# Optimization experiments

Measured on AMD Instinct MI355X. Metric: run time of the kernel, lower is better.

Reference implementation:

```python
import jax, jax.numpy as jnp
import numpy as np

B = 16384
OBS = 568        # 36 self features + 19 * 28 other-agent features
H = 256          # hidden_dim
SELF_DIM = 36
OTHER_DIM = 28
N_OTHER = (OBS - SELF_DIM) // OTHER_DIM  # 19


def _linear_init(key, fan_in, fan_out):
    # torch nn.Linear default: U(-1/sqrt(fan_in), 1/sqrt(fan_in))
    kw, kb = jax.random.split(key)
    s = 1.0 / np.sqrt(fan_in)
    W = jax.random.uniform(kw, (fan_in, fan_out), jnp.float32, -s, s)
    b = jax.random.uniform(kb, (fan_out,), jnp.float32, -s, s)
    return W, b


def setup_inputs() -> dict:
    key = jax.random.key(0)
    ks = jax.random.split(key, 10)
    x = jax.random.normal(ks[0], (B, OBS), jnp.float32)
    eps = jax.random.normal(ks[1], (B, H), jnp.float32)
    W_mu, b_mu = _linear_init(ks[2], OBS, H)
    W_var, b_var = _linear_init(ks[3], OBS, H)
    W_self, b_self = _linear_init(ks[4], SELF_DIM, H)
    W_other, b_other = _linear_init(ks[5], OTHER_DIM, H)
    W_q, b_q = _linear_init(ks[6], H, H)
    W_k, b_k = _linear_init(ks[7], H, H)
    W_v, b_v = _linear_init(ks[8], 2 * H, H)
    W_a, b_a = _linear_init(ks[9], 2 * H, H)
    return {"x": x, "eps": eps,
            "W_mu": W_mu, "b_mu": b_mu, "W_var": W_var, "b_var": b_var,
            "W_self": W_self, "b_self": b_self, "W_other": W_other, "b_other": b_other,
            "W_q": W_q, "b_q": b_q, "W_k": W_k, "b_k": b_k,
            "W_v": W_v, "b_v": b_v, "W_a": W_a, "b_a": b_a}


def reference(x, eps, W_mu, b_mu, W_var, b_var, W_self, b_self,
              W_other, b_other, W_q, b_q, W_k, b_k, W_v, b_v, W_a, b_a):
    relu = jax.nn.relu
    # VAE reparameterization (detach=False path)
    mu = x @ W_mu + b_mu                                  # [B, H]
    log_var = x @ W_var + b_var                           # [B, H]
    z = eps * jnp.exp(0.5 * log_var) + mu                 # [B, H]

    self_info = x[:, :SELF_DIM]                           # [B, 36]
    agents_info = x[:, SELF_DIM:].reshape(B, N_OTHER, OTHER_DIM)  # [B, N, 28]

    self_em = relu(self_info @ W_self + b_self)           # [B, H]
    other_ems = relu(agents_info @ W_other + b_other)     # [B, N, H]

    q = relu(z @ W_q + b_q)                               # [B, H]
    k = relu(other_ems @ W_k + b_k)                       # [B, N, H]
    v_in = jnp.concatenate(
        [other_ems, jnp.broadcast_to(self_em[:, None, :], (B, N_OTHER, H))], axis=-1)
    v = relu(v_in @ W_v + b_v)                            # [B, N, H]

    scores = jnp.einsum('bh,bnh->bn', q, k) / np.sqrt(H)  # [B, N]
    att_weight = jax.nn.softmax(scores, axis=-1)          # [B, N]
    h = jnp.einsum('bn,bnh->bh', att_weight, v)           # [B, H]

    out = relu(jnp.concatenate([h, self_em], axis=-1) @ W_a + b_a)  # [B, H]
    return out, att_weight[:, None, :]                    # att: [B, 1, N]
```

## Files before the change

### kernel.cpp

```cpp
#include <hip/hip_runtime.h>

typedef __bf16 bf16;
typedef __bf16 bf16x4 __attribute__((ext_vector_type(4)));
typedef __bf16 bf16x8 __attribute__((ext_vector_type(8)));
typedef float  f32x4  __attribute__((ext_vector_type(4)));

#define NB    16384
#define NOBS  568
#define NH    256
#define NAG   19

#define OFF_WT_MU    0u
#define OFF_WT_VAR   294912u
#define OFF_WT_SELF  589824u
#define OFF_WT_OTHER 622592u
#define OFF_WT_Q     638976u
#define OFF_WT_K     770048u
#define OFF_WT_V1    901120u
#define OFF_WT_V2    1032192u
#define OFF_WT_A1    1163264u
#define OFF_WT_A2    1294336u
#define OFF_Z        1425408u
#define OFF_SELF     9814016u
#define OFF_Q        18202624u
#define OFF_SV       26591232u
#define OFF_H        34979840u

static __device__ __forceinline__ unsigned short bfbits(float v) {
  bf16 b = (bf16)v;
  union { bf16 b; unsigned short u; } cvt; cvt.b = b; return cvt.u;
}

__global__ __launch_bounds__(256) void wprep(
    const float* __restrict__ Wmu, const float* __restrict__ Wvar,
    const float* __restrict__ Wself, const float* __restrict__ Wother,
    const float* __restrict__ Wq, const float* __restrict__ Wk,
    const float* __restrict__ Wv, const float* __restrict__ Wa, char* wsb)
{
  const float* src; bf16* dst; int K, Kp; bool chunked = false;
  switch (blockIdx.y) {
    case 0: src = Wmu;        dst = (bf16*)(wsb + OFF_WT_MU);    K = 568; Kp = 576; break;
    case 1: src = Wvar;       dst = (bf16*)(wsb + OFF_WT_VAR);   K = 568; Kp = 576; break;
    case 2: src = Wself;      dst = (bf16*)(wsb + OFF_WT_SELF);  K = 36;  Kp = 64;  break;
    case 3: src = Wother;     dst = (bf16*)(wsb + OFF_WT_OTHER); K = 28;  Kp = 32;  break;
    case 4: src = Wq;         dst = (bf16*)(wsb + OFF_WT_Q);     K = 256; Kp = 256; break;
    case 5: src = Wk;         dst = (bf16*)(wsb + OFF_WT_K);     K = 256; Kp = 256; chunked = true; break;
    case 6: src = Wv;         dst = (bf16*)(wsb + OFF_WT_V1);    K = 256; Kp = 256; chunked = true; break;
    case 7: src = Wv + 65536; dst = (bf16*)(wsb + OFF_WT_V2);    K = 256; Kp = 256; break;
    case 8: src = Wa;         dst = (bf16*)(wsb + OFF_WT_A1);    K = 256; Kp = 256; break;
    default: src = Wa + 65536; dst = (bf16*)(wsb + OFF_WT_A2);   K = 256; Kp = 256; break;
  }
  int total = 256 * Kp;
  if (chunked) {
    for (int i = blockIdx.x * 256 + threadIdx.x; i < total; i += gridDim.x * 256) {
      int ch = i >> 13, n = (i >> 5) & 255, kk = i & 31;
      int k = ch * 32 + kk;
      dst[i] = (bf16)src[k * 256 + n];
    }
  } else {
    for (int i = blockIdx.x * 256 + threadIdx.x; i < total; i += gridDim.x * 256) {
      int n = i / Kp, k = i - n * Kp;
      dst[i] = (k < K) ? (bf16)src[k * 256 + n] : (bf16)0.f;
    }
  }
}

template<int EMODE, bool AF32>
__global__ __launch_bounds__(256, 2) void gemm_k(
    const void* __restrict__ Aptr, const void* __restrict__ A2ptr,
    int lda, int K, int Klimit,
    const bf16* __restrict__ Wt, const bf16* __restrict__ Wt2,
    const float* __restrict__ bias, const float* __restrict__ bias2,
    const float* __restrict__ epsp, void* __restrict__ outp)
{
  constexpr bool DUALB = (EMODE == 0);
  constexpr bool DUALA = (EMODE == 3);
  __shared__ bf16 ldsA[64 * 40];
  __shared__ bf16 ldsB[128 * 40];
  __shared__ bf16 ldsB2[DUALB ? 128 * 40 : 8];

  const int tid = threadIdx.x;
  const int wave = tid >> 6;
  const int lane = tid & 63;
  const int quad = lane >> 4;
  const int m = lane & 15;
  const int rowbase = blockIdx.x * 64;
  const int colbase = blockIdx.y * 128;

  f32x4 acc[8];
  f32x4 accB[DUALB ? 8 : 1];
  const f32x4 z4 = {0.f, 0.f, 0.f, 0.f};
#pragma unroll
  for (int ct = 0; ct < 8; ++ct) acc[ct] = z4;
  if constexpr (DUALB) {
#pragma unroll
    for (int ct = 0; ct < 8; ++ct) accB[ct] = z4;
  }

  const int npass = DUALA ? 2 : 1;
  for (int pass = 0; pass < npass; ++pass) {
    const void* Ap = (pass == 0) ? Aptr : A2ptr;
    const bf16* Wp = (pass == 0) ? Wt : Wt2;
    for (int kc = 0; kc < K; kc += 32) {
      __syncthreads();
      if constexpr (AF32) {
        const float* Af = (const float*)Ap;
#pragma unroll
        for (int it = 0; it < 2; ++it) {
          int p = tid + 256 * it;
          int r = p >> 3, fs = p & 7;
          int k = kc + fs * 4;
          const float* src = Af + (size_t)(rowbase + r) * lda + k;
          float v0, v1, v2, v3;
          if (k + 4 <= Klimit) {
            float4 v = *(const float4*)src;
            v0 = v.x; v1 = v.y; v2 = v.z; v3 = v.w;
          } else {
            v0 = (k + 0 < Klimit) ? src[0] : 0.f;
            v1 = (k + 1 < Klimit) ? src[1] : 0.f;
            v2 = (k + 2 < Klimit) ? src[2] : 0.f;
            v3 = (k + 3 < Klimit) ? src[3] : 0.f;
          }
          bf16x4 o = {(bf16)v0, (bf16)v1, (bf16)v2, (bf16)v3};
          *(bf16x4*)(ldsA + r * 40 + fs * 4) = o;
        }
      } else {
        const bf16* Ab = (const bf16*)Ap;
        {
          int p = tid;
          int r = p >> 2, f = p & 3;
          *(bf16x8*)(ldsA + r * 40 + f * 8) =
              *(const bf16x8*)(Ab + (size_t)(rowbase + r) * lda + kc + f * 8);
        }
      }
#pragma unroll
      for (int it = 0; it < 2; ++it) {
        int p = tid + 256 * it;
        int n = p >> 2, f = p & 3;
        *(bf16x8*)(ldsB + n * 40 + f * 8) =
            *(const bf16x8*)(Wt + (size_t)(colbase + n) * K + kc + f * 8);
      }
      if constexpr (DUALB) {
#pragma unroll
        for (int it = 0; it < 2; ++it) {
          int p = tid + 256 * it;
          int n = p >> 2, f = p & 3;
          *(bf16x8*)(ldsB2 + n * 40 + f * 8) =
              *(const bf16x8*)(Wt2 + (size_t)(colbase + n) * K + kc + f * 8);
        }
      }
      __syncthreads();
      bf16x8 afrag = *(const bf16x8*)(ldsA + (wave * 16 + m) * 40 + quad * 8);
#pragma unroll
      for (int ct = 0; ct < 8; ++ct) {
        bf16x8 bfrag = *(const bf16x8*)(ldsB + (ct * 16 + m) * 40 + quad * 8);
        acc[ct] = __builtin_amdgcn_mfma_f32_16x16x32_bf16(afrag, bfrag, acc[ct], 0, 0, 0);
        if constexpr (DUALB) {
          bf16x8 b2 = *(const bf16x8*)(ldsB2 + (ct * 16 + m) * 40 + quad * 8);
          accB[ct] = __builtin_amdgcn_mfma_f32_16x16x32_bf16(afrag, b2, accB[ct], 0, 0, 0);
        }
      }
      (void)Wp;
    }
  }
#pragma unroll
  for (int ct = 0; ct < 8; ++ct) {
    const int col = colbase + ct * 16 + m;
    const float bv = bias[col];
#pragma unroll
    for (int r = 0; r < 4; ++r) {
      const size_t row = (size_t)rowbase + wave * 16 + quad * 4 + r;
      float v = acc[ct][r] + bv;
      if constexpr (EMODE == 0) {
        float lv = accB[ct][r] + bias2[col];
        float zz = epsp[row * 256 + col] * __expf(0.5f * lv) + v;
        ((bf16*)outp)[row * 256 + col] = (bf16)zz;
      } else if constexpr (EMODE == 1) {
        ((bf16*)outp)[row * 256 + col] = (bf16)(v > 0.f ? v : 0.f);
      } else if constexpr (EMODE == 2) {
        ((bf16*)outp)[row * 256 + col] = (bf16)v;
      } else {
        ((float*)outp)[row * 256 + col] = (v > 0.f ? v : 0.f);
      }
    }
  }
}

template<bool UNUSED>
__global__ __launch_bounds__(256, 2) void gemm_dualA(
    const bf16* __restrict__ A1, const bf16* __restrict__ A2,
    const bf16* __restrict__ Wt1, const bf16* __restrict__ Wt2,
    const float* __restrict__ bias, float* __restrict__ outp)
{
  __shared__ bf16 ldsA[64 * 40];
  __shared__ bf16 ldsB[128 * 40];

  const int tid = threadIdx.x;
  const int wave = tid >> 6;
  const int lane = tid & 63;
  const int quad = lane >> 4;
  const int m = lane & 15;
  const int rowbase = blockIdx.x * 64;
  const int colbase = blockIdx.y * 128;

  f32x4 acc[8];
  const f32x4 z4 = {0.f, 0.f, 0.f, 0.f};
#pragma unroll
  for (int ct = 0; ct < 8; ++ct) acc[ct] = z4;

  for (int pass = 0; pass < 2; ++pass) {
    const bf16* Ap = (pass == 0) ? A1 : A2;
    const bf16* Wp = (pass == 0) ? Wt1 : Wt2;
    for (int kc = 0; kc < 256; kc += 32) {
      __syncthreads();
      {
        int p = tid;
        int r = p >> 2, f = p & 3;
        *(bf16x8*)(ldsA + r * 40 + f * 8) =
            *(const bf16x8*)(Ap + (size_t)(rowbase + r) * 256 + kc + f * 8);
      }
#pragma unroll
      for (int it = 0; it < 2; ++it) {
        int p = tid + 256 * it;
        int n = p >> 2, f = p & 3;
        *(bf16x8*)(ldsB + n * 40 + f * 8) =
            *(const bf16x8*)(Wp + (size_t)(colbase + n) * 256 + kc + f * 8);
      }
      __syncthreads();
      bf16x8 afrag = *(const bf16x8*)(ldsA + (wave * 16 + m) * 40 + quad * 8);
#pragma unroll
      for (int ct = 0; ct < 8; ++ct) {
        bf16x8 bfrag = *(const bf16x8*)(ldsB + (ct * 16 + m) * 40 + quad * 8);
        acc[ct] = __builtin_amdgcn_mfma_f32_16x16x32_bf16(afrag, bfrag, acc[ct], 0, 0, 0);
      }
    }
  }
#pragma unroll
  for (int ct = 0; ct < 8; ++ct) {
    const int col = colbase + ct * 16 + m;
    const float bv = bias[col];
#pragma unroll
    for (int r = 0; r < 4; ++r) {
      const size_t row = (size_t)rowbase + wave * 16 + quad * 4 + r;
      float v = acc[ct][r] + bv;
      outp[row * 256 + col] = (v > 0.f ? v : 0.f);
    }
  }
}

__global__ __launch_bounds__(256, 3) void k_fused(
    const float* __restrict__ x, const bf16* __restrict__ qb,
    const bf16* __restrict__ svb,
    const bf16* __restrict__ WtOther, const float* __restrict__ b_other,
    const bf16* __restrict__ WtKc, const float* __restrict__ b_k,
    const bf16* __restrict__ WtVc,
    float* __restrict__ att_out, bf16* __restrict__ hb)
{
  __shared__ bf16 ldsO[80 * 264];
  __shared__ bf16 ldsA1[80 * 40];
  __shared__ bf16 qh16[1024];
  __shared__ bf16 svl16[1024];
  float* spart = (float*)ldsA1;
  float* attl  = (float*)ldsA1 + 320;

  const int tid = threadIdx.x, wave = tid >> 6, lane = tid & 63;
  const int quad = lane >> 4, m = lane & 15;
  const int b0 = blockIdx.x * 4;

  for (int i = tid; i < 512; i += 256) {
    ((unsigned*)qh16)[i]  = ((const unsigned*)(qb  + (size_t)b0 * 256))[i];
    ((unsigned*)svl16)[i] = ((const unsigned*)(svb + (size_t)b0 * 256))[i];
  }
  for (int i = tid; i < 80 * 16; i += 256) {
    int r = i >> 4, kk = (i & 15) * 2;
    float v0 = 0.f, v1 = 0.f;
    if (r < 76) {
      int bb = b0 + r / 19, n = r % 19;
      const float* base = x + (size_t)bb * NOBS + 36 + n * 28;
      if (kk < 28) v0 = base[kk];
      if (kk + 1 < 28) v1 = base[kk + 1];
    }
    unsigned u0 = bfbits(v0), u1 = bfbits(v1);
    *(unsigned*)(ldsA1 + r * 40 + kk) = u0 | (u1 << 16);
  }
  __syncthreads();

  const f32x4 z4 = {0.f, 0.f, 0.f, 0.f};

  {
    f32x4 acc1[5][4];
    bf16x8 bfr[4];
#pragma unroll
    for (int c = 0; c < 4; ++c)
      bfr[c] = *(const bf16x8*)(WtOther + ((4 * wave + c) * 16 + m) * 32 + quad * 8);
#pragma unroll
    for (int rt = 0; rt < 5; ++rt) {
      bf16x8 a = *(const bf16x8*)(ldsA1 + (rt * 16 + m) * 40 + quad * 8);
#pragma unroll
      for (int c = 0; c < 4; ++c)
        acc1[rt][c] = __builtin_amdgcn_mfma_f32_16x16x32_bf16(a, bfr[c], z4, 0, 0, 0);
    }
#pragma unroll
    for (int rt = 0; rt < 5; ++rt)
#pragma unroll
      for (int c = 0; c < 4; ++c) {
        int col = (4 * wave + c) * 16 + m;
        float bv = b_other[col];
#pragma unroll
        for (int r = 0; r < 4; ++r) {
          float v = acc1[rt][c][r] + bv;
          v = v > 0.f ? v : 0.f;
          unsigned u = bfbits(v);
          unsigned other = (unsigned)__shfl_xor((int)u, 1, 64);
          if ((m & 1) == 0) {
            int rowl = rt * 16 + quad * 4 + r;
            *(unsigned*)(ldsO + rowl * 264 + col) = u | (other << 16);
          }
        }
      }
  }
  __syncthreads();

  {
    f32x4 aK[5][4];
#pragma unroll
    for (int rt = 0; rt < 5; ++rt)
#pragma unroll
      for (int c = 0; c < 4; ++c) aK[rt][c] = z4;

#pragma unroll 1
    for (int ch = 0; ch < 8; ++ch) {
      const int kc = ch * 32;
      bf16x8 bK[4];
#pragma unroll
      for (int c = 0; c < 4; ++c)
        bK[c] = *(const bf16x8*)(WtKc + (size_t)ch * 8192 + ((4 * wave + c) * 16 + m) * 32 + quad * 8);
#pragma unroll
      for (int rt = 0; rt < 5; ++rt) {
        bf16x8 a = *(const bf16x8*)(ldsO + (rt * 16 + m) * 264 + kc + quad * 8);
#pragma unroll
        for (int c = 0; c < 4; ++c)
          aK[rt][c] = __builtin_amdgcn_mfma_f32_16x16x32_bf16(a, bK[c], aK[rt][c], 0, 0, 0);
      }
    }

#pragma unroll
    for (int rt = 0; rt < 5; ++rt) {
      float part[4] = {0.f, 0.f, 0.f, 0.f};
#pragma unroll
      for (int c = 0; c < 4; ++c) {
        int col = (4 * wave + c) * 16 + m;
        float bkv = b_k[col];
#pragma unroll
        for (int r = 0; r < 4; ++r) {
          int rowl = rt * 16 + quad * 4 + r;
          int br = rowl / 19; int bs = br > 3 ? 3 : br;
          float kv = aK[rt][c][r] + bkv;
          kv = kv > 0.f ? kv : 0.f;
          part[r] += kv * (float)qh16[bs * 256 + col];
        }
      }
#pragma unroll
      for (int r = 0; r < 4; ++r) {
        float p = part[r];
        p += __shfl_xor(p, 1, 64);
        p += __shfl_xor(p, 2, 64);
        p += __shfl_xor(p, 4, 64);
        p += __shfl_xor(p, 8, 64);
        if (m == 0) spart[wave * 80 + rt * 16 + quad * 4 + r] = p;
      }
    }
  }
  __syncthreads();
  if (tid < 4) {
    float sc[19];
    float mx = -1e30f;
#pragma unroll
    for (int j = 0; j < 19; ++j) {
      int row = tid * 19 + j;
      float s = (spart[row] + spart[80 + row] + spart[160 + row] + spart[240 + row]) * 0.0625f;
      sc[j] = s; mx = fmaxf(mx, s);
    }
    float sum = 0.f;
#pragma unroll
    for (int j = 0; j < 19; ++j) { float e = __expf(sc[j] - mx); sc[j] = e; sum += e; }
    float inv = 1.f / sum;
#pragma unroll
    for (int j = 0; j < 19; ++j) {
      float a = sc[j] * inv;
      attl[tid * 19 + j] = a;
      att_out[(size_t)(b0 + tid) * 19 + j] = a;
    }
  }
  __syncthreads();

  {
    f32x4 aV[5][4];
#pragma unroll
    for (int rt = 0; rt < 5; ++rt)
#pragma unroll
      for (int c = 0; c < 4; ++c) aV[rt][c] = z4;

#pragma unroll 1
    for (int ch = 0; ch < 8; ++ch) {
      const int kc = ch * 32;
      bf16x8 bV[4];
#pragma unroll
      for (int c = 0; c < 4; ++c)
        bV[c] = *(const bf16x8*)(WtVc + (size_t)ch * 8192 + ((4 * wave + c) * 16 + m) * 32 + quad * 8);
#pragma unroll
      for (int rt = 0; rt < 5; ++rt) {
        bf16x8 a = *(const bf16x8*)(ldsO + (rt * 16 + m) * 264 + kc + quad * 8);
#pragma unroll
        for (int c = 0; c < 4; ++c)
          aV[rt][c] = __builtin_amdgcn_mfma_f32_16x16x32_bf16(a, bV[c], aV[rt][c], 0, 0, 0);
      }
    }

    float hacc[4][4];
#pragma unroll
    for (int c = 0; c < 4; ++c)
#pragma unroll
      for (int bb = 0; bb < 4; ++bb) hacc[c][bb] = 0.f;
#pragma unroll
    for (int rt = 0; rt < 5; ++rt)
#pragma unroll
      for (int c = 0; c < 4; ++c) {
        int col = (4 * wave + c) * 16 + m;
#pragma unroll
        for (int r = 0; r < 4; ++r) {
          int rowl = rt * 16 + quad * 4 + r;
          int br = rowl / 19; int bs = br > 3 ? 3 : br;
          float v = aV[rt][c][r] + (float)svl16[bs * 256 + col];
          v = v > 0.f ? v : 0.f;
          int ai = bs * 19 + (rowl - bs * 19);
          float hv = v * attl[ai < 76 ? ai : 75];
#pragma unroll
          for (int bb = 0; bb < 4; ++bb)
            hacc[c][bb] += (br == bb) ? hv : 0.f;
        }
      }
    __syncthreads();
#pragma unroll
    for (int c = 0; c < 4; ++c)
#pragma unroll
      for (int bb = 0; bb < 4; ++bb) {
        float h = hacc[c][bb];
        h += __shfl_xor(h, 16, 64);
        h += __shfl_xor(h, 32, 64);
        if (quad == 0) qh16[bb * 256 + (4 * wave + c) * 16 + m] = (bf16)h;
      }
  }
  __syncthreads();
  for (int i = tid; i < 512; i += 256)
    ((unsigned*)(hb + (size_t)b0 * 256))[i] = ((const unsigned*)qh16)[i];
}

extern "C" void kernel_launch(void* const* d_in, const int* in_sizes, int n_in,
                              void* d_out, int out_size, void* d_ws, size_t ws_size,
                              hipStream_t stream) {
  (void)in_sizes; (void)n_in; (void)out_size; (void)ws_size;
  const float* x      = (const float*)d_in[0];
  const float* eps    = (const float*)d_in[1];
  const float* W_mu   = (const float*)d_in[2];
  const float* b_mu   = (const float*)d_in[3];
  const float* W_var  = (const float*)d_in[4];
  const float* b_var  = (const float*)d_in[5];
  const float* W_self = (const float*)d_in[6];
  const float* b_self = (const float*)d_in[7];
  const float* W_other= (const float*)d_in[8];
  const float* b_other= (const float*)d_in[9];
  const float* W_q    = (const float*)d_in[10];
  const float* b_q    = (const float*)d_in[11];
  const float* W_k    = (const float*)d_in[12];
  const float* b_k    = (const float*)d_in[13];
  const float* W_v    = (const float*)d_in[14];
  const float* b_v    = (const float*)d_in[15];
  const float* W_a    = (const float*)d_in[16];
  const float* b_a    = (const float*)d_in[17];

  char* wsb = (char*)d_ws;
  bf16* WtMu    = (bf16*)(wsb + OFF_WT_MU);
  bf16* WtVar   = (bf16*)(wsb + OFF_WT_VAR);
  bf16* WtSelf  = (bf16*)(wsb + OFF_WT_SELF);
  bf16* WtOther = (bf16*)(wsb + OFF_WT_OTHER);
  bf16* WtQ     = (bf16*)(wsb + OFF_WT_Q);
  bf16* WtK     = (bf16*)(wsb + OFF_WT_K);
  bf16* WtV1    = (bf16*)(wsb + OFF_WT_V1);
  bf16* WtV2    = (bf16*)(wsb + OFF_WT_V2);
  bf16* WtA1    = (bf16*)(wsb + OFF_WT_A1);
  bf16* WtA2    = (bf16*)(wsb + OFF_WT_A2);
  bf16* zbuf    = (bf16*)(wsb + OFF_Z);
  bf16* selfbuf = (bf16*)(wsb + OFF_SELF);
  bf16* qbuf    = (bf16*)(wsb + OFF_Q);
  bf16* svbuf   = (bf16*)(wsb + OFF_SV);
  bf16* hbuf    = (bf16*)(wsb + OFF_H);

  float* out = (float*)d_out;
  float* att_out = out + (size_t)NB * 256;

  dim3 blk(256);
  dim3 ggrid(NB / 64, 2);
  wprep<<<dim3(160, 10), blk, 0, stream>>>(W_mu, W_var, W_self, W_other, W_q, W_k, W_v, W_a, wsb);
  gemm_k<0, true><<<ggrid, blk, 0, stream>>>(x, nullptr, 568, 576, 568,
                                             WtMu, WtVar, b_mu, b_var, eps, zbuf);
  gemm_k<1, true><<<ggrid, blk, 0, stream>>>(x, nullptr, 568, 64, 568,
                                             WtSelf, nullptr, b_self, nullptr, nullptr, selfbuf);
  gemm_k<1, false><<<ggrid, blk, 0, stream>>>(zbuf, nullptr, 256, 256, 256,
                                              WtQ, nullptr, b_q, nullptr, nullptr, qbuf);
  gemm_k<2, false><<<ggrid, blk, 0, stream>>>(selfbuf, nullptr, 256, 256, 256,
                                              WtV2, nullptr, b_v, nullptr, nullptr, svbuf);
  k_fused<<<NB / 4, blk, 0, stream>>>(x, qbuf, svbuf, WtOther, b_other, WtK, b_k,
                                      WtV1, att_out, hbuf);
  gemm_dualA<true><<<ggrid, blk, 0, stream>>>(hbuf, selfbuf, WtA1, WtA2, b_a, out);
}
```

Measured before the change: 347.6 us.

## Merge independent GEMM launches and reorder agent rows in fused attention kernel

Merges the z and self-embedding GEMMs into one launch, and the q and self-value GEMMs into another, using blockIdx.y to select the branch. This cuts two kernel launches and lets the independent GEMMs share one grid. In the fused attention kernel, agent rows are reordered so that row = agent*4 + batch. That lets q, self-value, biases and attention weights sit in registers per lane and removes the per-element division by 19 and the masked accumulation. It also prefetches the next K/V weight chunk while the current one is computed. Costs are branch divergence in the merged GEMMs, load imbalance between K=576 and K=64 blocks, and higher register pressure.

```diff
diff --git a/kernel.cpp b/kernel.cpp
--- a/kernel.cpp
+++ b/kernel.cpp
@@ -65,19 +65,17 @@
   }
 }
 
-template<int EMODE, bool AF32>
-__global__ __launch_bounds__(256, 2) void gemm_k(
-    const void* __restrict__ Aptr, const void* __restrict__ A2ptr,
-    int lda, int K, int Klimit,
-    const bf16* __restrict__ Wt, const bf16* __restrict__ Wt2,
-    const float* __restrict__ bias, const float* __restrict__ bias2,
-    const float* __restrict__ epsp, void* __restrict__ outp)
+__global__ __launch_bounds__(256, 3) void gemm_zself(
+    const float* __restrict__ x,
+    const bf16* __restrict__ WtMu, const bf16* __restrict__ WtVar,
+    const bf16* __restrict__ WtSelf,
+    const float* __restrict__ b_mu, const float* __restrict__ b_var,
+    const float* __restrict__ b_self, const float* __restrict__ eps,
+    bf16* __restrict__ zout, bf16* __restrict__ selfout)
 {
-  constexpr bool DUALB = (EMODE == 0);
-  constexpr bool DUALA = (EMODE == 3);
   __shared__ bf16 ldsA[64 * 40];
   __shared__ bf16 ldsB[128 * 40];
-  __shared__ bf16 ldsB2[DUALB ? 128 * 40 : 8];
+  __shared__ bf16 ldsB2[128 * 40];
 
   const int tid = threadIdx.x;
   const int wave = tid >> 6;
@@ -85,82 +83,66 @@
   const int quad = lane >> 4;
   const int m = lane & 15;
   const int rowbase = blockIdx.x * 64;
-  const int colbase = blockIdx.y * 128;
-
-  f32x4 acc[8];
-  f32x4 accB[DUALB ? 8 : 1];
+  const int colbase = (blockIdx.y & 1) * 128;
+  const bool isZ = blockIdx.y < 2;
+  const int K = isZ ? 576 : 64;
+  const bf16* __restrict__ Wt = isZ ? WtMu : WtSelf;
+  const float* __restrict__ bias = isZ ? b_mu : b_self;
+
+  f32x4 acc[8], accB[8];
   const f32x4 z4 = {0.f, 0.f, 0.f, 0.f};
 #pragma unroll
-  for (int ct = 0; ct < 8; ++ct) acc[ct] = z4;
-  if constexpr (DUALB) {
-#pragma unroll
-    for (int ct = 0; ct < 8; ++ct) accB[ct] = z4;
-  }
-
-  const int npass = DUALA ? 2 : 1;
-  for (int pass = 0; pass < npass; ++pass) {
-    const void* Ap = (pass == 0) ? Aptr : A2ptr;
-    const bf16* Wp = (pass == 0) ? Wt : Wt2;
-    for (int kc = 0; kc < K; kc += 32) {
-      __syncthreads();
-      if constexpr (AF32) {
-        const float* Af = (const float*)Ap;
-#pragma unroll
-        for (int it = 0; it < 2; ++it) {
-          int p = tid + 256 * it;
-          int r = p >> 3, fs = p & 7;
-          int k = kc + fs * 4;
-          const float* src = Af + (size_t)(rowbase + r) * lda + k;
-          float v0, v1, v2, v3;
-          if (k + 4 <= Klimit) {
-            float4 v = *(const float4*)src;
-            v0 = v.x; v1 = v.y; v2 = v.z; v3 = v.w;
-          } else {
-            v0 = (k + 0 < Klimit) ? src[0] : 0.f;
-            v1 = (k + 1 < Klimit) ? src[1] : 0.f;
-            v2 = (k + 2 < Klimit) ? src[2] : 0.f;
-            v3 = (k + 3 < Klimit) ? src[3] : 0.f;
-          }
-          bf16x4 o = {(bf16)v0, (bf16)v1, (bf16)v2, (bf16)v3};
-          *(bf16x4*)(ldsA + r * 40 + fs * 4) = o;
+  for (int ct = 0; ct < 8; ++ct) { acc[ct] = z4; accB[ct] = z4; }
+
+  for (int kc = 0; kc < K; kc += 32) {
+    __syncthreads();
+    {
+#pragma unroll
+      for (int it = 0; it < 2; ++it) {
+        int p = tid + 256 * it;
+        int r = p >> 3, fs = p & 7;
+        int k = kc + fs * 4;
+        const float* src = x + (size_t)(rowbase + r) * 568 + k;
+        float v0, v1, v2, v3;
+        if (k + 4 <= 568) {
+          float4 v = *(const float4*)src;
+          v0 = v.x; v1 = v.y; v2 = v.z; v3 = v.w;
+        } else {
+          v0 = (k + 0 < 568) ? src[0] : 0.f;
+          v1 = (k + 1 < 568) ? src[1] : 0.f;
+          v2 = (k + 2 < 568) ? src[2] : 0.f;
+          v3 = (k + 3 < 568) ? src[3] : 0.f;
         }
-      } else {
-        const bf16* Ab = (const bf16*)Ap;
-        {
-          int p = tid;
-          int r = p >> 2, f = p & 3;
-          *(bf16x8*)(ldsA + r * 40 + f * 8) =
-              *(const bf16x8*)(Ab + (size_t)(rowbase + r) * lda + kc + f * 8);
-        }
-      }
+        bf16x4 o = {(bf16)v0, (bf16)v1, (bf16)v2, (bf16)v3};
+        *(bf16x4*)(ldsA + r * 40 + fs * 4) = o;
+      }
+    }
+#pragma unroll
+    for (int it = 0; it < 2; ++it) {
+      int p = tid + 256 * it;
+      int n = p >> 2, f = p & 3;
+      *(bf16x8*)(ldsB + n * 40 + f * 8) =
+          *(const bf16x8*)(Wt + (size_t)(colbase + n) * K + kc + f * 8);
+    }
+    if (isZ) {
 #pragma unroll
       for (int it = 0; it < 2; ++it) {
         int p = tid + 256 * it;
         int n = p >> 2, f = p & 3;
-        *(bf16x8*)(ldsB + n * 40 + f * 8) =
-            *(const bf16x8*)(Wt + (size_t)(colbase + n) * K + kc + f * 8);
-      }
-      if constexpr (DUALB) {
-#pragma unroll
-        for (int it = 0; it < 2; ++it) {
-          int p = tid + 256 * it;
-          int n = p >> 2, f = p & 3;
-          *(bf16x8*)(ldsB2 + n * 40 + f * 8) =
-              *(const bf16x8*)(Wt2 + (size_t)(colbase + n) * K + kc + f * 8);
-        }
-      }
-      __syncthreads();
-      bf16x8 afrag = *(const bf16x8*)(ldsA + (wave * 16 + m) * 40 + quad * 8);
-#pragma unroll
-      for (int ct = 0; ct < 8; ++ct) {
-        bf16x8 bfrag = *(const bf16x8*)(ldsB + (ct * 16 + m) * 40 + quad * 8);
-        acc[ct] = __builtin_amdgcn_mfma_f32_16x16x32_bf16(afrag, bfrag, acc[ct], 0, 0, 0);
-        if constexpr (DUALB) {
-          bf16x8 b2 = *(const bf16x8*)(ldsB2 + (ct * 16 + m) * 40 + quad * 8);
-          accB[ct] = __builtin_amdgcn_mfma_f32_16x16x32_bf16(afrag, b2, accB[ct], 0, 0, 0);
-        }
-      }
-      (void)Wp;
+        *(bf16x8*)(ldsB2 + n * 40 + f * 8) =
+            *(const bf16x8*)(WtVar + (size_t)(colbase + n) * 576 + kc + f * 8);
+      }
+    }
+    __syncthreads();
+    bf16x8 afrag = *(const bf16x8*)(ldsA + (wave * 16 + m) * 40 + quad * 8);
+#pragma unroll
+    for (int ct = 0; ct < 8; ++ct) {
+      bf16x8 bfrag = *(const bf16x8*)(ldsB + (ct * 16 + m) * 40 + quad * 8);
+      acc[ct] = __builtin_amdgcn_mfma_f32_16x16x32_bf16(afrag, bfrag, acc[ct], 0, 0, 0);
+      if (isZ) {
+        bf16x8 b2 = *(const bf16x8*)(ldsB2 + (ct * 16 + m) * 40 + quad * 8);
+        accB[ct] = __builtin_amdgcn_mfma_f32_16x16x32_bf16(afrag, b2, accB[ct], 0, 0, 0);
+      }
     }
   }
 #pragma unroll
@@ -171,17 +153,77 @@
     for (int r = 0; r < 4; ++r) {
       const size_t row = (size_t)rowbase + wave * 16 + quad * 4 + r;
       float v = acc[ct][r] + bv;
-      if constexpr (EMODE == 0) {
-        float lv = accB[ct][r] + bias2[col];
-        float zz = epsp[row * 256 + col] * __expf(0.5f * lv) + v;
-        ((bf16*)outp)[row * 256 + col] = (bf16)zz;
-      } else if constexpr (EMODE == 1) {
-        ((bf16*)outp)[row * 256 + col] = (bf16)(v > 0.f ? v : 0.f);
-      } else if constexpr (EMODE == 2) {
-        ((bf16*)outp)[row * 256 + col] = (bf16)v;
+      if (isZ) {
+        float lv = accB[ct][r] + b_var[col];
+        float zz = eps[row * 256 + col] * __expf(0.5f * lv) + v;
+        zout[row * 256 + col] = (bf16)zz;
       } else {
-        ((float*)outp)[row * 256 + col] = (v > 0.f ? v : 0.f);
-      }
+        selfout[row * 256 + col] = (bf16)(v > 0.f ? v : 0.f);
+      }
+    }
+  }
+}
+
+__global__ __launch_bounds__(256, 4) void gemm_qsv(
+    const bf16* __restrict__ zb, const bf16* __restrict__ selfb,
+    const bf16* __restrict__ WtQ, const bf16* __restrict__ WtV2,
+    const float* __restrict__ b_q, const float* __restrict__ b_v,
+    bf16* __restrict__ qout, bf16* __restrict__ svout)
+{
+  __shared__ bf16 ldsA[64 * 40];
+  __shared__ bf16 ldsB[128 * 40];
+
+  const int tid = threadIdx.x;
+  const int wave = tid >> 6;
+  const int lane = tid & 63;
+  const int quad = lane >> 4;
+  const int m = lane & 15;
+  const int rowbase = blockIdx.x * 64;
+  const int colbase = (blockIdx.y & 1) * 128;
+  const bool isQ = blockIdx.y < 2;
+  const bf16* __restrict__ Ap = isQ ? zb : selfb;
+  const bf16* __restrict__ Wt = isQ ? WtQ : WtV2;
+  const float* __restrict__ bias = isQ ? b_q : b_v;
+  bf16* __restrict__ outp = isQ ? qout : svout;
+
+  f32x4 acc[8];
+  const f32x4 z4 = {0.f, 0.f, 0.f, 0.f};
+#pragma unroll
+  for (int ct = 0; ct < 8; ++ct) acc[ct] = z4;
+
+  for (int kc = 0; kc < 256; kc += 32) {
+    __syncthreads();
+    {
+      int p = tid;
+      int r = p >> 2, f = p & 3;
+      *(bf16x8*)(ldsA + r * 40 + f * 8) =
+          *(const bf16x8*)(Ap + (size_t)(rowbase + r) * 256 + kc + f * 8);
+    }
+#pragma unroll
+    for (int it = 0; it < 2; ++it) {
+      int p = tid + 256 * it;
+      int n = p >> 2, f = p & 3;
+      *(bf16x8*)(ldsB + n * 40 + f * 8) =
+          *(const bf16x8*)(Wt + (size_t)(colbase + n) * 256 + kc + f * 8);
+    }
+    __syncthreads();
+    bf16x8 afrag = *(const bf16x8*)(ldsA + (wave * 16 + m) * 40 + quad * 8);
+#pragma unroll
+    for (int ct = 0; ct < 8; ++ct) {
+      bf16x8 bfrag = *(const bf16x8*)(ldsB + (ct * 16 + m) * 40 + quad * 8);
+      acc[ct] = __builtin_amdgcn_mfma_f32_16x16x32_bf16(afrag, bfrag, acc[ct], 0, 0, 0);
+    }
+  }
+#pragma unroll
+  for (int ct = 0; ct < 8; ++ct) {
+    const int col = colbase + ct * 16 + m;
+    const float bv = bias[col];
+#pragma unroll
+    for (int r = 0; r < 4; ++r) {
+      const size_t row = (size_t)rowbase + wave * 16 + quad * 4 + r;
+      float v = acc[ct][r] + bv;
+      if (isQ) v = (v > 0.f ? v : 0.f);
+      outp[row * 256 + col] = (bf16)v;
     }
   }
 }
@@ -273,10 +315,10 @@
   }
   for (int i = tid; i < 80 * 16; i += 256) {
     int r = i >> 4, kk = (i & 15) * 2;
+    int n = r >> 2, bb = r & 3;
     float v0 = 0.f, v1 = 0.f;
-    if (r < 76) {
-      int bb = b0 + r / 19, n = r % 19;
-      const float* base = x + (size_t)bb * NOBS + 36 + n * 28;
+    if (n < 19) {
+      const float* base = x + (size_t)(b0 + bb) * NOBS + 36 + n * 28;
       if (kk < 28) v0 = base[kk];
       if (kk + 1 < 28) v1 = base[kk + 1];
     }
@@ -288,6 +330,9 @@
   const f32x4 z4 = {0.f, 0.f, 0.f, 0.f};
 
   {
+    float bo[4];
+#pragma unroll
+    for (int c = 0; c < 4; ++c) bo[c] = b_other[(4 * wave + c) * 16 + m];
     f32x4 acc1[5][4];
     bf16x8 bfr[4];
 #pragma unroll
@@ -305,10 +350,9 @@
 #pragma unroll
       for (int c = 0; c < 4; ++c) {
         int col = (4 * wave + c) * 16 + m;
-        float bv = b_other[col];
 #pragma unroll
         for (int r = 0; r < 4; ++r) {
-          float v = acc1[rt][c][r] + bv;
+          float v = acc1[rt][c][r] + bo[c];
           v = v > 0.f ? v : 0.f;
           unsigned u = bfbits(v);
           unsigned other = (unsigned)__shfl_xor((int)u, 1, 64);
@@ -321,6 +365,17 @@
   }
   __syncthreads();
 
+  float qreg[4][4];
+#pragma unroll
+  for (int c = 0; c < 4; ++c) {
+    int col = (4 * wave + c) * 16 + m;
+#pragma unroll
+    for (int r = 0; r < 4; ++r) qreg[c][r] = (float)qh16[r * 256 + col];
+  }
+  float bkreg[4];
+#pragma unroll
+  for (int c = 0; c < 4; ++c) bkreg[c] = b_k[(4 * wave + c) * 16 + m];
+
   {
     f32x4 aK[5][4];
 #pragma unroll
@@ -328,13 +383,19 @@
 #pragma unroll
       for (int c = 0; c < 4; ++c) aK[rt][c] = z4;
 
+    bf16x8 bK[4];
+#pragma unroll
+    for (int c = 0; c < 4; ++c)
+      bK[c] = *(const bf16x8*)(WtKc + ((4 * wave + c) * 16 + m) * 32 + quad * 8);
 #pragma unroll 1
     for (int ch = 0; ch < 8; ++ch) {
+      bf16x8 bN[4];
+      if (ch < 7) {
+#pragma unroll
+        for (int c = 0; c < 4; ++c)
+          bN[c] = *(const bf16x8*)(WtKc + (size_t)(ch + 1) * 8192 + ((4 * wave + c) * 16 + m) * 32 + quad * 8);
+      }
       const int kc = ch * 32;
-      bf16x8 bK[4];
-#pragma unroll
-      for (int c = 0; c < 4; ++c)
-        bK[c] = *(const bf16x8*)(WtKc + (size_t)ch * 8192 + ((4 * wave + c) * 16 + m) * 32 + quad * 8);
 #pragma unroll
       for (int rt = 0; rt < 5; ++rt) {
         bf16x8 a = *(const bf16x8*)(ldsO + (rt * 16 + m) * 264 + kc + quad * 8);
@@ -342,6 +403,10 @@
         for (int c = 0; c < 4; ++c)
           aK[rt][c] = __builtin_amdgcn_mfma_f32_16x16x32_bf16(a, bK[c], aK[rt][c], 0, 0, 0);
       }
+      if (ch < 7) {
+#pragma unroll
+        for (int c = 0; c < 4; ++c) bK[c] = bN[c];
+      }
     }
 
 #pragma unroll
@@ -349,15 +414,11 @@
       float part[4] = {0.f, 0.f, 0.f, 0.f};
 #pragma unroll
       for (int c = 0; c < 4; ++c) {
-        int col = (4 * wave + c) * 16 + m;
-        float bkv = b_k[col];
 #pragma unroll
         for (int r = 0; r < 4; ++r) {
-          int rowl = rt * 16 + quad * 4 + r;
-          int br = rowl / 19; int bs = br > 3 ? 3 : br;
-          float kv = aK[rt][c][r] + bkv;
+          float kv = aK[rt][c][r] + bkreg[c];
           kv = kv > 0.f ? kv : 0.f;
-          part[r] += kv * (float)qh16[bs * 256 + col];
+          part[r] += kv * qreg[c][r];
         }
       }
 #pragma unroll
@@ -377,7 +438,7 @@
     float mx = -1e30f;
 #pragma unroll
     for (int j = 0; j < 19; ++j) {
-      int row = tid * 19 + j;
+      int row = j * 4 + tid;
       float s = (spart[row] + spart[80 + row] + spart[160 + row] + spart[240 + row]) * 0.0625f;
       sc[j] = s; mx = fmaxf(mx, s);
     }
@@ -388,11 +449,20 @@
 #pragma unroll
     for (int j = 0; j < 19; ++j) {
       float a = sc[j] * inv;
-      attl[tid * 19 + j] = a;
+      attl[j * 4 + tid] = a;
       att_out[(size_t)(b0 + tid) * 19 + j] = a;
     }
+    attl[76 + tid] = 0.f;
   }
   __syncthreads();
+
+  float svreg[4][4];
+#pragma unroll
+  for (int c = 0; c < 4; ++c) {
+    int col = (4 * wave + c) * 16 + m;
+#pragma unroll
+    for (int r = 0; r < 4; ++r) svreg[c][r] = (float)svl16[r * 256 + col];
+  }
 
   {
     f32x4 aV[5][4];
@@ -401,13 +471,19 @@
 #pragma unroll
       for (int c = 0; c < 4; ++c) aV[rt][c] = z4;
 
+    bf16x8 bV[4];
+#pragma unroll
+    for (int c = 0; c < 4; ++c)
+      bV[c] = *(const bf16x8*)(WtVc + ((4 * wave + c) * 16 + m) * 32 + quad * 8);
 #pragma unroll 1
     for (int ch = 0; ch < 8; ++ch) {
+      bf16x8 bN[4];
+      if (ch < 7) {
+#pragma unroll
+        for (int c = 0; c < 4; ++c)
+          bN[c] = *(const bf16x8*)(WtVc + (size_t)(ch + 1) * 8192 + ((4 * wave + c) * 16 + m) * 32 + quad * 8);
+      }
       const int kc = ch * 32;
-      bf16x8 bV[4];
-#pragma unroll
-      for (int c = 0; c < 4; ++c)
-        bV[c] = *(const bf16x8*)(WtVc + (size_t)ch * 8192 + ((4 * wave + c) * 16 + m) * 32 + quad * 8);
 #pragma unroll
       for (int rt = 0; rt < 5; ++rt) {
         bf16x8 a = *(const bf16x8*)(ldsO + (rt * 16 + m) * 264 + kc + quad * 8);
@@ -415,40 +491,40 @@
         for (int c = 0; c < 4; ++c)
           aV[rt][c] = __builtin_amdgcn_mfma_f32_16x16x32_bf16(a, bV[c], aV[rt][c], 0, 0, 0);
       }
+      if (ch < 7) {
+#pragma unroll
+        for (int c = 0; c < 4; ++c) bV[c] = bN[c];
+      }
     }
 
     float hacc[4][4];
 #pragma unroll
     for (int c = 0; c < 4; ++c)
 #pragma unroll
-      for (int bb = 0; bb < 4; ++bb) hacc[c][bb] = 0.f;
-#pragma unroll
-    for (int rt = 0; rt < 5; ++rt)
+      for (int r = 0; r < 4; ++r) hacc[c][r] = 0.f;
+#pragma unroll
+    for (int rt = 0; rt < 5; ++rt) {
+      float av[4];
+#pragma unroll
+      for (int r = 0; r < 4; ++r) av[r] = attl[rt * 16 + quad * 4 + r];
 #pragma unroll
       for (int c = 0; c < 4; ++c) {
-        int col = (4 * wave + c) * 16 + m;
 #pragma unroll
         for (int r = 0; r < 4; ++r) {
-          int rowl = rt * 16 + quad * 4 + r;
-          int br = rowl / 19; int bs = br > 3 ? 3 : br;
-          float v = aV[rt][c][r] + (float)svl16[bs * 256 + col];
+          float v = aV[rt][c][r] + svreg[c][r];
           v = v > 0.f ? v : 0.f;
-          int ai = bs * 19 + (rowl - bs * 19);
-          float hv = v * attl[ai < 76 ? ai : 75];
-#pragma unroll
-          for (int bb = 0; bb < 4; ++bb)
-            hacc[c][bb] += (br == bb) ? hv : 0.f;
+          hacc[c][r] += v * av[r];
         }
       }
-    __syncthreads();
+    }
 #pragma unroll
     for (int c = 0; c < 4; ++c)
 #pragma unroll
-      for (int bb = 0; bb < 4; ++bb) {
-        float h = hacc[c][bb];
+      for (int r = 0; r < 4; ++r) {
+        float h = hacc[c][r];
         h += __shfl_xor(h, 16, 64);
         h += __shfl_xor(h, 32, 64);
-        if (quad == 0) qh16[bb * 256 + (4 * wave + c) * 16 + m] = (bf16)h;
+        if (quad == 0) qh16[r * 256 + (4 * wave + c) * 16 + m] = (bf16)h;
       }
   }
   __syncthreads();
@@ -500,17 +576,12 @@
   float* att_out = out + (size_t)NB * 256;
 
   dim3 blk(256);
-  dim3 ggrid(NB / 64, 2);
   wprep<<<dim3(160, 10), blk, 0, stream>>>(W_mu, W_var, W_self, W_other, W_q, W_k, W_v, W_a, wsb);
-  gemm_k<0, true><<<ggrid, blk, 0, stream>>>(x, nullptr, 568, 576, 568,
-                                             WtMu, WtVar, b_mu, b_var, eps, zbuf);
-  gemm_k<1, true><<<ggrid, blk, 0, stream>>>(x, nullptr, 568, 64, 568,
-                                             WtSelf, nullptr, b_self, nullptr, nullptr, selfbuf);
-  gemm_k<1, false><<<ggrid, blk, 0, stream>>>(zbuf, nullptr, 256, 256, 256,
-                                              WtQ, nullptr, b_q, nullptr, nullptr, qbuf);
-  gemm_k<2, false><<<ggrid, blk, 0, stream>>>(selfbuf, nullptr, 256, 256, 256,
-                                              WtV2, nullptr, b_v, nullptr, nullptr, svbuf);
+  gemm_zself<<<dim3(NB / 64, 4), blk, 0, stream>>>(x, WtMu, WtVar, WtSelf,
+                                                   b_mu, b_var, b_self, eps, zbuf, selfbuf);
+  gemm_qsv<<<dim3(NB / 64, 4), blk, 0, stream>>>(zbuf, selfbuf, WtQ, WtV2,
+                                                 b_q, b_v, qbuf, svbuf);
   k_fused<<<NB / 4, blk, 0, stream>>>(x, qbuf, svbuf, WtOther, b_other, WtK, b_k,
                                       WtV1, att_out, hbuf);
-  gemm_dualA<true><<<ggrid, blk, 0, stream>>>(hbuf, selfbuf, WtA1, WtA2, b_a, out);
-}
+  gemm_dualA<true><<<dim3(NB / 64, 2), blk, 0, stream>>>(hbuf, selfbuf, WtA1, WtA2, b_a, out);
+}
```

Measured after the change: 338.1 us. 1.03x faster.
